# Kernel optimization log

Hardware: AMD Instinct MI355X
Metric: run time of the kernel (lower is better)

The kernel has to match this reference:

```python
import jax, jax.numpy as jnp
import numpy as np

EPS = 1e-5
M = 8          # num_modules
NUM_LAYERS = 4


def gumbel_softmax(logits, u, tau):
    g = -jnp.log(-jnp.log(jnp.clip(u, 1e-10, 1.0 - 1e-7)))
    return jax.nn.softmax((logits + g) / tau, axis=-1)


def batchnorm(x, gamma, beta):
    # training-mode BN over batch axis 0; x: [B, ...], gamma/beta broadcast over trailing dims
    mean = jnp.mean(x, axis=0, keepdims=True)
    var = jnp.mean(jnp.square(x - mean), axis=0, keepdims=True)  # biased var, as torch BN
    return (x - mean) * jax.lax.rsqrt(var + EPS) * gamma + beta


def setup_inputs() -> dict:
    key = jax.random.key(0)
    ks = jax.random.split(key, 32)
    B = 16384
    d = {}
    d['x'] = jax.random.normal(ks[0], (B, 128), jnp.float32)
    d['embedding_input'] = jax.random.normal(ks[1], (B, 128), jnp.float32)
    d['u_sel'] = jax.random.uniform(ks[2], (B, NUM_LAYERS - 1, M, M), jnp.float32)
    d['u_final'] = jax.random.uniform(ks[3], (B, M), jnp.float32)
    shapes = [('base_W0', (128, 400)), ('base_b0', (400,)), ('base_W1', (400, 256)), ('base_b1', (256,)),
              ('em_W0', (128, 400)), ('em_b0', (400,)),
              ('gat_W0', (400, 256)), ('gat_b0', (256,)), ('gat_W1', (256, 256)), ('gat_b1', (256,)),
              ('sel_W', (3, 256, 64)), ('sel_b', (3, 64)), ('selF_W', (256, 8)), ('selF_b', (8,)),
              ('cond_W', (3, 64, 256)), ('cond_b', (3, 256)),
              ('mod_W', (8, 256, 256)), ('mod_b', (8, 256)),
              ('last_W', (256, 18)), ('last_b', (18,))]
    for i, (name, sh) in enumerate(shapes):
        fan_in = sh[-2] if len(sh) >= 2 else sh[-1]
        d[name] = jax.random.normal(ks[4 + i], sh, jnp.float32) / np.sqrt(fan_in)
    d['bn1_g'] = jnp.ones((8, 256), jnp.float32)
    d['bn1_b'] = jnp.zeros((8, 256), jnp.float32)
    d['bn2_g'] = jnp.ones((8, 256), jnp.float32)
    d['bn2_b'] = jnp.zeros((8, 256), jnp.float32)
    return d


def forward(x, embedding_input, u_sel, u_final,
            base_W0, base_b0, base_W1, base_b1, em_W0, em_b0,
            gat_W0, gat_b0, gat_W1, gat_b1,
            sel_W, sel_b, selF_W, selF_b, cond_W, cond_b,
            mod_W, mod_b, bn1_g, bn1_b, bn2_g, bn2_b, last_W, last_b):
    relu = jax.nn.relu
    # base MLP (last activation is identity)
    h = relu(x @ base_W0 + base_b0)
    out = h @ base_W1 + base_b1                       # [B, 256]
    # embedding base (single layer, identity last activation)
    emb = embedding_input @ em_W0 + em_b0             # [B, 400]
    # gating fcs: activation THEN fc, per source loop
    emb = relu(emb) @ gat_W0 + gat_b0
    emb = relu(emb) @ gat_W1 + gat_b1                 # [B, 256]

    # routing logits (stochastic branch, tau = select_temp = 1.0)
    select_input = relu(emb)
    gsels = []
    for i in range(NUM_LAYERS - 1):
        logit = jnp.tanh(select_input @ sel_W[i] + sel_b[i])       # [B, 64]
        sraw = logit.reshape(logit.shape[0], M, M)                  # [B, M, M]
        gsels.append(gumbel_softmax(sraw, u_sel[:, i], 1.0))
        select_input = relu((logit @ cond_W[i] + cond_b[i]) * emb)
    final_select = gumbel_softmax(select_input @ selF_W + selF_b, u_final, 1.0)  # [B, M]
    # selects were insert(0, ...)'d in torch -> consumed in reversed order
    selects = gsels[::-1]

    # layer-0 expert modules: BN -> Linear -> BN (only layers[0] is used in forward)
    mean = jnp.mean(out, axis=0, keepdims=True)
    var = jnp.mean(jnp.square(out - mean), axis=0, keepdims=True)
    xhat = (out - mean) * jax.lax.rsqrt(var + EPS)                  # shared normalization
    t = xhat[:, None, :] * bn1_g + bn1_b                            # [B, M, 256] per-module affine
    h = jnp.einsum('bmd,mdh->bmh', t, mod_W) + mod_b                # [B, M, 256]
    prev = batchnorm(h, bn2_g, bn2_b)                               # [B, M, 256]

    # cascade: weighted combination + relu per layer
    for l in range(NUM_LAYERS - 1):
        prev = relu(jnp.einsum('bmk,bkh->bmh', selects[l], prev))
    out = jnp.einsum('bm,bmh->bh', final_select, prev)              # [B, 256]
    return out @ last_W + last_b                                    # [B, 18]


def reference(x, embedding_input, u_sel, u_final,
              base_W0, base_b0, base_W1, base_b1, em_W0, em_b0,
              gat_W0, gat_b0, gat_W1, gat_b1,
              sel_W, sel_b, selF_W, selF_b, cond_W, cond_b,
              mod_W, mod_b, bn1_g, bn1_b, bn2_g, bn2_b, last_W, last_b):
    return forward(x, embedding_input, u_sel, u_final,
                   base_W0, base_b0, base_W1, base_b1, em_W0, em_b0,
                   gat_W0, gat_b0, gat_W1, gat_b1,
                   sel_W, sel_b, selF_W, selF_b, cond_W, cond_b,
                   mod_W, mod_b, bn1_g, bn1_b, bn2_g, bn2_b, last_W, last_b)
```

## Files before the change

### kernel.cpp

```cpp
#include <hip/hip_runtime.h>
#include <math.h>


typedef short bf16x8 __attribute__((ext_vector_type(8)));
typedef float f32x4 __attribute__((ext_vector_type(4)));

__device__ __forceinline__ unsigned short f2bf(float f) {
  unsigned u = __float_as_uint(f);
  u += 0x7fffu + ((u >> 16) & 1u);
  return (unsigned short)(u >> 16);
}
__device__ __forceinline__ float bf2f(unsigned short h) {
  return __uint_as_float(((unsigned)h) << 16);
}
__device__ __forceinline__ unsigned pack2(float a, float b) {
  return ((unsigned)f2bf(b) << 16) | f2bf(a);
}
__device__ __forceinline__ void gload_lds16(const void* g, void* l) {
  __builtin_amdgcn_global_load_lds(
      (const __attribute__((address_space(1))) unsigned int*)g,
      (__attribute__((address_space(3))) unsigned int*)l, 16, 0, 0);
}
__device__ __forceinline__ bf16x8 relu_bf8(bf16x8 v) {
  bf16x8 r;
  #pragma unroll
  for (int j = 0; j < 8; ++j) r[j] = v[j] > 0 ? v[j] : (short)0;
  return r;
}

#define EPI_NONE  0
#define EPI_RELU  1
#define EPI_STATS 4

__global__ __launch_bounds__(256) void prep_all(
    const float* __restrict__ base_W0, const float* __restrict__ em_W0,
    const float* __restrict__ base_W1, const float* __restrict__ gat_W0,
    const float* __restrict__ gat_W1, const float* __restrict__ sel_W,
    const float* __restrict__ cond_W, const float* __restrict__ last_W,
    unsigned short* __restrict__ W0t, unsigned short* __restrict__ emW0t,
    unsigned short* __restrict__ W1t, unsigned short* __restrict__ g0t,
    unsigned short* __restrict__ g1t, unsigned short* __restrict__ selWt,
    unsigned short* __restrict__ condWt, unsigned short* __restrict__ lastWt,
    float* __restrict__ stats)
{
  __shared__ float t[32][33];
  int bid = blockIdx.x;
  const int tid = threadIdx.x;
  const int tx = tid & 31, ty = tid >> 5;

  if (bid < 496) {
    const float* src; unsigned short* dst; int K, N, KP, gx, local;
    if (bid < 64)       { src = base_W0; dst = W0t;   K = 128; N = 400; KP = 128; gx = 4;  local = bid; }
    else if (bid < 128) { src = em_W0;   dst = emW0t; K = 128; N = 400; KP = 128; gx = 4;  local = bid - 64; }
    else if (bid < 232) { src = base_W1; dst = W1t;   K = 400; N = 256; KP = 416; gx = 13; local = bid - 128; }
    else if (bid < 336) { src = gat_W0;  dst = g0t;   K = 400; N = 256; KP = 416; gx = 13; local = bid - 232; }
    else if (bid < 400) { src = gat_W1;  dst = g1t;   K = 256; N = 256; KP = 256; gx = 8;  local = bid - 336; }
    else if (bid < 448) {
      const int i = (bid - 400) / 16;
      src = sel_W + i * 16384; dst = selWt + i * 16384;
      K = 256; N = 64; KP = 256; gx = 8; local = (bid - 400) % 16;
    } else {
      const int i = (bid - 448) / 16;
      src = cond_W + i * 16384; dst = condWt + i * 16384;
      K = 64; N = 256; KP = 64; gx = 2; local = (bid - 448) % 16;
    }
    const int k0 = (local % gx) * 32, n0 = (local / gx) * 32;
    #pragma unroll
    for (int p = 0; p < 4; ++p) {
      const int k = k0 + ty + p * 8;
      t[ty + p * 8][tx] = (k < K && n0 + tx < N) ? src[(size_t)k * N + n0 + tx] : 0.f;
    }
    __syncthreads();
    #pragma unroll
    for (int p = 0; p < 4; ++p) {
      const int n = n0 + ty + p * 8;
      dst[(size_t)n * KP + k0 + tx] = f2bf(t[tx][ty + p * 8]);
    }
    return;
  }
  bid -= 496;

  if (bid < 8) {
    const int k0 = bid * 32;
    #pragma unroll
    for (int p = 0; p < 4; ++p)
      t[ty + p * 8][tx] = (tx < 18) ? last_W[(size_t)(k0 + ty + p * 8) * 18 + tx] : 0.f;
    __syncthreads();
    #pragma unroll
    for (int p = 0; p < 4; ++p) {
      const int n = ty + p * 8;
      lastWt[(size_t)n * 256 + k0 + tx] = f2bf(t[tx][n]);
      lastWt[(size_t)(n + 32) * 256 + k0 + tx] = 0;
    }
    return;
  }

  for (int i = tid; i < 4608; i += 256) stats[i] = 0.f;
}

__global__ __launch_bounds__(256) void gemm_w0(
    const float* __restrict__ Ax, const float* __restrict__ Ae,
    const unsigned short* __restrict__ Wx, const unsigned short* __restrict__ We,
    const float* __restrict__ bx, const float* __restrict__ be,
    unsigned short* __restrict__ Cx, unsigned short* __restrict__ Ce)
{
  __shared__ unsigned short As[128 * 32];
  __shared__ unsigned short Bs[128 * 32];
  const float* Ap = blockIdx.z ? Ae : Ax;
  const unsigned short* Wp = blockIdx.z ? We : Wx;
  const float* bp = blockIdx.z ? be : bx;
  unsigned short* Cp = blockIdx.z ? Ce : Cx;
  const int row0 = blockIdx.y * 128;
  const int n0 = blockIdx.x * 128;
  const int tid = threadIdx.x;
  const int wid = tid >> 6, lane = tid & 63;
  const int wr = wid >> 1, wc = wid & 1;
  const int arow = tid >> 2, kcol = (tid & 3) * 8;
  const int lr = lane & 15, lk = (lane >> 4) * 8;
  const int lrow = (lane >> 4) * 4;

  f32x4 acc[4][4] = {};
  for (int k0 = 0; k0 < 128; k0 += 32) {
    {
      const float4* s1 = reinterpret_cast<const float4*>(
          Ap + (size_t)(row0 + arow) * 128 + k0 + kcol);
      uint4 w1 = {pack2(s1[0].x, s1[0].y), pack2(s1[0].z, s1[0].w),
                  pack2(s1[1].x, s1[1].y), pack2(s1[1].z, s1[1].w)};
      *reinterpret_cast<uint4*>(&As[arow * 32 + kcol]) = w1;
      const float4* s2 = reinterpret_cast<const float4*>(
          Ap + (size_t)(row0 + 64 + arow) * 128 + k0 + kcol);
      uint4 w2 = {pack2(s2[0].x, s2[0].y), pack2(s2[0].z, s2[0].w),
                  pack2(s2[1].x, s2[1].y), pack2(s2[1].z, s2[1].w)};
      *reinterpret_cast<uint4*>(&As[(64 + arow) * 32 + kcol]) = w2;
    }
    gload_lds16(Wp + (size_t)(n0 + arow) * 128 + k0 + kcol, (char*)Bs + tid * 16);
    gload_lds16(Wp + (size_t)(n0 + 64 + arow) * 128 + k0 + kcol,
                (char*)Bs + 4096 + tid * 16);
    __syncthreads();
    bf16x8 a[4], b[4];
    #pragma unroll
    for (int i = 0; i < 4; ++i)
      a[i] = *reinterpret_cast<const bf16x8*>(&As[(wr * 64 + i * 16 + lr) * 32 + lk]);
    #pragma unroll
    for (int j = 0; j < 4; ++j)
      b[j] = *reinterpret_cast<const bf16x8*>(&Bs[(wc * 64 + j * 16 + lr) * 32 + lk]);
    #pragma unroll
    for (int i = 0; i < 4; ++i)
      #pragma unroll
      for (int j = 0; j < 4; ++j)
        acc[i][j] = __builtin_amdgcn_mfma_f32_16x16x32_bf16(a[i], b[j], acc[i][j], 0, 0, 0);
    __syncthreads();
  }
  #pragma unroll
  for (int j = 0; j < 4; ++j) {
    const int col = n0 + wc * 64 + j * 16 + lr;
    if (col >= 416) continue;
    const bool real = col < 400;
    const float bv = real ? bp[col] : 0.f;
    #pragma unroll
    for (int i = 0; i < 4; ++i) {
      #pragma unroll
      for (int r = 0; r < 4; ++r) {
        const int row = row0 + wr * 64 + i * 16 + lrow + r;
        float v = real ? fmaxf(acc[i][j][r] + bv, 0.f) : 0.f;
        Cp[(size_t)row * 416 + col] = f2bf(v);
      }
    }
  }
}

template<int BN, int WM, int WN, int EPI, bool RELU_A>
__global__ __launch_bounds__(256) void gemm_bf16(
    const unsigned short* __restrict__ A, int AS,
    const unsigned short* __restrict__ Wt, const float* __restrict__ bias,
    unsigned short* __restrict__ C, int CS, int Nreal, int NP, int K,
    const unsigned short* __restrict__ emb,
    float* __restrict__ sum, float* __restrict__ sumsq)
{
  constexpr int FRAG_M = 128 / WM / 16;
  constexpr int FRAG_N = BN / WN / 16;
  __shared__ unsigned short As[128 * 32];
  __shared__ unsigned short Bs[BN * 32];
  const int row0 = blockIdx.y * 128;
  const int n0 = blockIdx.x * BN;
  const int tid = threadIdx.x;
  const int wid = tid >> 6, lane = tid & 63;
  const int wr = wid / WN, wc = wid % WN;
  const int arow = tid >> 2;
  const int kcol = (tid & 3) * 8;
  const int lr = lane & 15, lk = (lane >> 4) * 8;
  const int lrow = (lane >> 4) * 4;

  f32x4 acc[FRAG_M][FRAG_N] = {};
  for (int k0 = 0; k0 < K; k0 += 32) {
    gload_lds16(A + (size_t)(row0 + arow) * AS + k0 + kcol, (char*)As + tid * 16);
    gload_lds16(A + (size_t)(row0 + 64 + arow) * AS + k0 + kcol, (char*)As + 4096 + tid * 16);
    gload_lds16(Wt + (size_t)(n0 + arow) * K + k0 + kcol, (char*)Bs + tid * 16);
    if constexpr (BN == 128)
      gload_lds16(Wt + (size_t)(n0 + 64 + arow) * K + k0 + kcol, (char*)Bs + 4096 + tid * 16);
    __syncthreads();
    bf16x8 a[FRAG_M], b[FRAG_N];
    #pragma unroll
    for (int i = 0; i < FRAG_M; ++i) {
      a[i] = *reinterpret_cast<const bf16x8*>(&As[(wr * (128 / WM) + i * 16 + lr) * 32 + lk]);
      if (RELU_A) a[i] = relu_bf8(a[i]);
    }
    #pragma unroll
    for (int j = 0; j < FRAG_N; ++j)
      b[j] = *reinterpret_cast<const bf16x8*>(&Bs[(wc * (BN / WN) + j * 16 + lr) * 32 + lk]);
    #pragma unroll
    for (int i = 0; i < FRAG_M; ++i)
      #pragma unroll
      for (int j = 0; j < FRAG_N; ++j)
        acc[i][j] = __builtin_amdgcn_mfma_f32_16x16x32_bf16(a[i], b[j], acc[i][j], 0, 0, 0);
    __syncthreads();
  }
  #pragma unroll
  for (int j = 0; j < FRAG_N; ++j) {
    const int col = n0 + wc * (BN / WN) + j * 16 + lr;
    if (col >= NP) continue;
    const bool real = col < Nreal;
    const float bv = real ? bias[col] : 0.f;
    float s = 0.f, q = 0.f;
    #pragma unroll
    for (int i = 0; i < FRAG_M; ++i) {
      #pragma unroll
      for (int r = 0; r < 4; ++r) {
        const int row = row0 + wr * (128 / WM) + i * 16 + lrow + r;
        float v = acc[i][j][r] + bv;
        if (EPI == EPI_RELU) v = fmaxf(v, 0.f);
        if (!real) v = 0.f;
        const unsigned short hv = f2bf(v);
        C[(size_t)row * CS + col] = hv;
        if (EPI == EPI_STATS) {
          const float vr = bf2f(hv);
          s += vr;
          q = fmaf(vr, vr, q);
        }
      }
    }
    if (EPI == EPI_STATS) {
      s += __shfl_xor(s, 16); s += __shfl_xor(s, 32);
      q += __shfl_xor(q, 16); q += __shfl_xor(q, 32);
      if (lane < 16) {
        atomicAdd(&sum[col], s);
        atomicAdd(&sumsq[col], q);
      }
    }
  }
}

__global__ __launch_bounds__(256) void gemm_mod(
    const unsigned short* __restrict__ A,
    const unsigned short* __restrict__ Wt,
    const float* __restrict__ bias, unsigned short* __restrict__ C,
    float* __restrict__ sum, float* __restrict__ sumsq)
{
  __shared__ unsigned short As[128 * 32];
  __shared__ unsigned short Bs[128 * 32];
  const int lin = blockIdx.x;
  const int swz = (lin & 7) * 256 + (lin >> 3);
  const int row0 = (swz >> 4) * 128;
  const int n0 = (swz & 15) * 128;
  const int tid = threadIdx.x;
  const int wid = tid >> 6, lane = tid & 63;
  const int wr = wid >> 1, wc = wid & 1;
  const int arow = tid >> 2;
  const int kcol = (tid & 3) * 8;
  const int lr = lane & 15, lk = (lane >> 4) * 8;
  const int lrow = (lane >> 4) * 4;

  f32x4 acc[4][4] = {};
  for (int k0 = 0; k0 < 256; k0 += 32) {
    gload_lds16(A + (size_t)(row0 + arow) * 256 + k0 + kcol, (char*)As + tid * 16);
    gload_lds16(A + (size_t)(row0 + 64 + arow) * 256 + k0 + kcol, (char*)As + 4096 + tid * 16);
    gload_lds16(Wt + (size_t)(n0 + arow) * 256 + k0 + kcol, (char*)Bs + tid * 16);
    gload_lds16(Wt + (size_t)(n0 + 64 + arow) * 256 + k0 + kcol, (char*)Bs + 4096 + tid * 16);
    __syncthreads();
    bf16x8 a[4], b[4];
    #pragma unroll
    for (int i = 0; i < 4; ++i)
      a[i] = *reinterpret_cast<const bf16x8*>(&As[(wr * 64 + i * 16 + lr) * 32 + lk]);
    #pragma unroll
    for (int j = 0; j < 4; ++j)
      b[j] = *reinterpret_cast<const bf16x8*>(&Bs[(wc * 64 + j * 16 + lr) * 32 + lk]);
    #pragma unroll
    for (int i = 0; i < 4; ++i)
      #pragma unroll
      for (int j = 0; j < 4; ++j)
        acc[i][j] = __builtin_amdgcn_mfma_f32_16x16x32_bf16(a[i], b[j], acc[i][j], 0, 0, 0);
    __syncthreads();
  }
  #pragma unroll
  for (int j = 0; j < 4; ++j) {
    const int col = n0 + wc * 64 + j * 16 + lr;
    const float bv = bias[col];
    float s = 0.f, q = 0.f;
    #pragma unroll
    for (int i = 0; i < 4; ++i) {
      #pragma unroll
      for (int r = 0; r < 4; ++r) {
        const int row = row0 + wr * 64 + i * 16 + lrow + r;
        const unsigned short hv = f2bf(acc[i][j][r] + bv);
        C[(size_t)row * 2048 + col] = hv;
        const float vr = bf2f(hv);
        s += vr;
        q = fmaf(vr, vr, q);
      }
    }
    s += __shfl_xor(s, 16); s += __shfl_xor(s, 32);
    q += __shfl_xor(q, 16); q += __shfl_xor(q, 32);
    if (lane < 16) {
      atomicAdd(&sum[col], s);
      atomicAdd(&sumsq[col], q);
    }
  }
}

template<bool RELU_A>
__global__ __launch_bounds__(256) void fused_select(
    const unsigned short* __restrict__ A, const unsigned short* __restrict__ selWt,
    const float* __restrict__ selb, const unsigned short* __restrict__ condWt,
    const float* __restrict__ condb, const unsigned short* __restrict__ emb,
    const float* __restrict__ u, int u_off,
    float* __restrict__ gs, unsigned short* __restrict__ siout)
{
  __shared__ unsigned short As[128 * 32];
  __shared__ unsigned short Bs[64 * 32];
  __shared__ unsigned short Ls[128 * 72];
  const int tid = threadIdx.x;
  const int wid = tid >> 6, lane = tid & 63;
  const int lr = lane & 15, hi = lane >> 4;
  const int lk = hi * 8;
  const int row0 = blockIdx.x * 128;
  const int arow = tid >> 2, kcol = (tid & 3) * 8;

  {
    f32x4 acc[2][4] = {};
    for (int k0 = 0; k0 < 256; k0 += 32) {
      gload_lds16(A + (size_t)(row0 + arow) * 256 + k0 + kcol, (char*)As + tid * 16);
      gload_lds16(A + (size_t)(row0 + 64 + arow) * 256 + k0 + kcol, (char*)As + 4096 + tid * 16);
      gload_lds16(selWt + (size_t)arow * 256 + k0 + kcol, (char*)Bs + tid * 16);
      __syncthreads();
      bf16x8 a[2], b[4];
      #pragma unroll
      for (int i = 0; i < 2; ++i) {
        a[i] = *reinterpret_cast<const bf16x8*>(&As[(wid * 32 + i * 16 + lr) * 32 + lk]);
        if (RELU_A) a[i] = relu_bf8(a[i]);
      }
      #pragma unroll
      for (int j = 0; j < 4; ++j)
        b[j] = *reinterpret_cast<const bf16x8*>(&Bs[(j * 16 + lr) * 32 + lk]);
      #pragma unroll
      for (int i = 0; i < 2; ++i)
        #pragma unroll
        for (int j = 0; j < 4; ++j)
          acc[i][j] = __builtin_amdgcn_mfma_f32_16x16x32_bf16(a[i], b[j], acc[i][j], 0, 0, 0);
      __syncthreads();
    }
    #pragma unroll
    for (int j = 0; j < 4; ++j) {
      const int col = j * 16 + lr;
      const float bv = selb[col];
      #pragma unroll
      for (int i = 0; i < 2; ++i)
        #pragma unroll
        for (int r = 0; r < 4; ++r) {
          const int row = wid * 32 + i * 16 + hi * 4 + r;
          Ls[row * 72 + col] = f2bf(tanhf(acc[i][j][r] + bv));
        }
    }
  }
  __syncthreads();

  #pragma unroll
  for (int p = 0; p < 4; ++p) {
    const int pair = p * 256 + tid;
    const int bl = pair >> 3, mm = pair & 7;
    const int bg = row0 + bl;
    float v[8];
    #pragma unroll
    for (int jj = 0; jj < 8; ++jj) v[jj] = bf2f(Ls[bl * 72 + mm * 8 + jj]);
    const float* up = u + (size_t)bg * 192 + u_off + mm * 8;
    #pragma unroll
    for (int jj = 0; jj < 8; ++jj) {
      const float uu = fminf(fmaxf(up[jj], 1e-10f), 0.9999999f);
      v[jj] -= logf(-logf(uu));
    }
    float mx = v[0];
    #pragma unroll
    for (int jj = 1; jj < 8; ++jj) mx = fmaxf(mx, v[jj]);
    float s = 0.f;
    #pragma unroll
    for (int jj = 0; jj < 8; ++jj) { v[jj] = expf(v[jj] - mx); s += v[jj]; }
    const float inv = 1.f / s;
    float* op = gs + (size_t)bg * 64 + mm * 8;
    #pragma unroll
    for (int jj = 0; jj < 8; ++jj) op[jj] = v[jj] * inv;
  }

  {
    const int wr2 = wid >> 1, wc2 = wid & 1;
    f32x4 acc2[4][8] = {};
    #pragma unroll
    for (int kq = 0; kq < 2; ++kq) {
      const int k0 = kq * 32;
      bf16x8 a2[4];
      #pragma unroll
      for (int i = 0; i < 4; ++i)
        a2[i] = *reinterpret_cast<const bf16x8*>(
            &Ls[(wr2 * 64 + i * 16 + lr) * 72 + k0 + hi * 8]);
      #pragma unroll
      for (int j = 0; j < 8; ++j) {
        const bf16x8 b2 = *reinterpret_cast<const bf16x8*>(
            condWt + (size_t)(wc2 * 128 + j * 16 + lr) * 64 + k0 + hi * 8);
        #pragma unroll
        for (int i = 0; i < 4; ++i)
          acc2[i][j] = __builtin_amdgcn_mfma_f32_16x16x32_bf16(a2[i], b2, acc2[i][j], 0, 0, 0);
      }
    }
    #pragma unroll
    for (int j = 0; j < 8; ++j) {
      const int col = wc2 * 128 + j * 16 + lr;
      const float bv = condb[col];
      #pragma unroll
      for (int i = 0; i < 4; ++i)
        #pragma unroll
        for (int r = 0; r < 4; ++r) {
          const int row = row0 + wr2 * 64 + i * 16 + hi * 4 + r;
          float vv = (acc2[i][j][r] + bv) * bf2f(emb[(size_t)row * 256 + col]);
          siout[(size_t)row * 256 + col] = f2bf(fmaxf(vv, 0.f));
        }
    }
  }
}

__global__ void final_select_k(const unsigned short* __restrict__ si, const float* __restrict__ Wf,
                               const float* __restrict__ bias, const float* __restrict__ u,
                               float* __restrict__ fs)
{
  const int idx = blockIdx.x * 256 + threadIdx.x;
  const int b = idx >> 3, j = idx & 7;
  const unsigned short* sp = si + (size_t)b * 256;
  float acc = bias[j];
  for (int k = 0; k < 256; ++k) acc = fmaf(bf2f(sp[k]), Wf[k * 8 + j], acc);
  const float uu = fminf(fmaxf(u[(size_t)b * 8 + j], 1e-10f), 0.9999999f);
  float v = acc - logf(-logf(uu));
  float mx = v;
  #pragma unroll
  for (int d = 1; d < 8; d <<= 1) mx = fmaxf(mx, __shfl_xor(mx, d, 8));
  float e = expf(v - mx);
  float s = e;
  #pragma unroll
  for (int d = 1; d < 8; d <<= 1) s += __shfl_xor(s, d, 8);
  fs[(size_t)b * 8 + j] = e / s;
}

__global__ __launch_bounds__(256) void fold_modw_all(
    const float* __restrict__ W, const float* __restrict__ g1,
    const float* __restrict__ b1, const float* __restrict__ modb,
    const float* __restrict__ sum1, const float* __restrict__ sumsq1,
    unsigned short* __restrict__ Wt, float* __restrict__ bias2)
{
  const float invB = 1.f / 16384.f;
  if (blockIdx.z == 8) {
    if (blockIdx.y != 0) return;
    const int m = blockIdx.x, h = threadIdx.x;
    float acc = modb[m * 256 + h];
    for (int d = 0; d < 256; ++d) {
      const float mean = sum1[d] * invB;
      const float var = sumsq1[d] * invB - mean * mean;
      const float r = rsqrtf(var + 1e-5f);
      const float c = b1[m * 256 + d] - mean * r * g1[m * 256 + d];
      acc = fmaf(c, W[((size_t)m * 256 + d) * 256 + h], acc);
    }
    bias2[m * 256 + h] = acc;
    return;
  }
  __shared__ float t[32][33];
  const int m = blockIdx.z, d0 = blockIdx.y * 32, h0 = blockIdx.x * 32;
  const int tx = threadIdx.x & 31, ty = threadIdx.x >> 5;
  #pragma unroll
  for (int p = 0; p < 4; ++p) {
    const int d = d0 + ty + p * 8;
    const float mean = sum1[d] * invB;
    const float var = sumsq1[d] * invB - mean * mean;
    const float r = rsqrtf(var + 1e-5f);
    t[ty + p * 8][tx] = W[((size_t)m * 256 + d) * 256 + h0 + tx] * r * g1[m * 256 + d];
  }
  __syncthreads();
  #pragma unroll
  for (int p = 0; p < 4; ++p) {
    const int h = h0 + ty + p * 8;
    Wt[((size_t)m * 256 + h) * 256 + d0 + tx] = f2bf(t[tx][ty + p * 8]);
  }
}

__global__ void finalize_bn2(const float* __restrict__ sum, const float* __restrict__ sumsq,
                             const float* __restrict__ g, const float* __restrict__ b,
                             float* __restrict__ scale, float* __restrict__ shift)
{
  const int i = blockIdx.x * 256 + threadIdx.x;
  const float invB = 1.f / 16384.f;
  const float m = sum[i] * invB;
  const float v = sumsq[i] * invB - m * m;
  const float r = rsqrtf(v + 1e-5f);
  const float sc = r * g[i];
  scale[i] = sc;
  shift[i] = b[i] - m * sc;
}

__global__ __launch_bounds__(256) void final_cascade(
    const unsigned short* __restrict__ H, const float* __restrict__ scale2,
    const float* __restrict__ shift2, const float* __restrict__ gs0,
    const float* __restrict__ gs1, const float* __restrict__ gs2,
    const float* __restrict__ fs, unsigned short* __restrict__ ovec)
{
  const int wave = threadIdx.x >> 6, lane = threadIdx.x & 63;
  const int b = __builtin_amdgcn_readfirstlane(blockIdx.x * 4 + wave);
  const int c0 = lane << 2;

  float prev[8][4];
  #pragma unroll
  for (int m = 0; m < 8; ++m) {
    const int gc = m * 256 + c0;
    const ushort4 h = *reinterpret_cast<const ushort4*>(&H[(size_t)b * 2048 + gc]);
    const float4 sc = *reinterpret_cast<const float4*>(&scale2[gc]);
    const float4 sh = *reinterpret_cast<const float4*>(&shift2[gc]);
    prev[m][0] = bf2f(h.x) * sc.x + sh.x;
    prev[m][1] = bf2f(h.y) * sc.y + sh.y;
    prev[m][2] = bf2f(h.z) * sc.z + sh.z;
    prev[m][3] = bf2f(h.w) * sc.w + sh.w;
  }

  const float* sel0 = gs2 + (size_t)b * 64;
  const float* sel1 = gs1 + (size_t)b * 64;
  const float* sel2 = gs0 + (size_t)b * 64;
  #pragma unroll
  for (int l = 0; l < 3; ++l) {
    const float* sp = (l == 0) ? sel0 : (l == 1) ? sel1 : sel2;
    float nw[8][4];
    #pragma unroll
    for (int m = 0; m < 8; ++m) {
      float a0 = 0.f, a1 = 0.f, a2 = 0.f, a3 = 0.f;
      #pragma unroll
      for (int k = 0; k < 8; ++k) {
        const float s = sp[m * 8 + k];
        a0 = fmaf(s, prev[k][0], a0);
        a1 = fmaf(s, prev[k][1], a1);
        a2 = fmaf(s, prev[k][2], a2);
        a3 = fmaf(s, prev[k][3], a3);
      }
      nw[m][0] = fmaxf(a0, 0.f); nw[m][1] = fmaxf(a1, 0.f);
      nw[m][2] = fmaxf(a2, 0.f); nw[m][3] = fmaxf(a3, 0.f);
    }
    #pragma unroll
    for (int m = 0; m < 8; ++m)
      #pragma unroll
      for (int c = 0; c < 4; ++c)
        prev[m][c] = nw[m][c];
  }

  const float* fp = fs + (size_t)b * 8;
  float ov[4] = {0.f, 0.f, 0.f, 0.f};
  #pragma unroll
  for (int m = 0; m < 8; ++m) {
    const float s = fp[m];
    ov[0] = fmaf(s, prev[m][0], ov[0]);
    ov[1] = fmaf(s, prev[m][1], ov[1]);
    ov[2] = fmaf(s, prev[m][2], ov[2]);
    ov[3] = fmaf(s, prev[m][3], ov[3]);
  }
  ushort4 o;
  o.x = f2bf(ov[0]); o.y = f2bf(ov[1]); o.z = f2bf(ov[2]); o.w = f2bf(ov[3]);
  *reinterpret_cast<ushort4*>(&ovec[(size_t)b * 256 + c0]) = o;
}

__global__ __launch_bounds__(256) void gemm_last(
    const unsigned short* __restrict__ A, const unsigned short* __restrict__ Wt,
    const float* __restrict__ bias, float* __restrict__ out)
{
  __shared__ unsigned short As[128 * 32];
  __shared__ unsigned short Bs[64 * 32];
  const int row0 = blockIdx.y * 128;
  const int tid = threadIdx.x;
  const int wid = tid >> 6, lane = tid & 63;
  const int arow = tid >> 2;
  const int kcol = (tid & 3) * 8;
  const int lr = lane & 15, lk = (lane >> 4) * 8;
  const int lrow = (lane >> 4) * 4;

  f32x4 acc[2][4] = {};
  for (int k0 = 0; k0 < 256; k0 += 32) {
    gload_lds16(A + (size_t)(row0 + arow) * 256 + k0 + kcol, (char*)As + tid * 16);
    gload_lds16(A + (size_t)(row0 + 64 + arow) * 256 + k0 + kcol, (char*)As + 4096 + tid * 16);
    gload_lds16(Wt + (size_t)arow * 256 + k0 + kcol, (char*)Bs + tid * 16);
    __syncthreads();
    bf16x8 a[2], b[4];
    #pragma unroll
    for (int i = 0; i < 2; ++i)
      a[i] = *reinterpret_cast<const bf16x8*>(&As[(wid * 32 + i * 16 + lr) * 32 + lk]);
    #pragma unroll
    for (int j = 0; j < 4; ++j)
      b[j] = *reinterpret_cast<const bf16x8*>(&Bs[(j * 16 + lr) * 32 + lk]);
    #pragma unroll
    for (int i = 0; i < 2; ++i)
      #pragma unroll
      for (int j = 0; j < 4; ++j)
        acc[i][j] = __builtin_amdgcn_mfma_f32_16x16x32_bf16(a[i], b[j], acc[i][j], 0, 0, 0);
    __syncthreads();
  }
  #pragma unroll
  for (int j = 0; j < 2; ++j) {
    const int col = j * 16 + lr;
    if (col >= 18) continue;
    const float bv = bias[col];
    #pragma unroll
    for (int i = 0; i < 2; ++i) {
      #pragma unroll
      for (int r = 0; r < 4; ++r) {
        const int row = row0 + wid * 32 + i * 16 + lrow + r;
        out[(size_t)row * 18 + col] = acc[i][j][r] + bv;
      }
    }
  }
}

extern "C" void kernel_launch(void* const* d_in, const int* in_sizes, int n_in,
                              void* d_out, int out_size, void* d_ws, size_t ws_size,
                              hipStream_t stream)
{
  (void)in_sizes; (void)n_in; (void)out_size; (void)ws_size;
  const float* x       = (const float*)d_in[0];
  const float* embi    = (const float*)d_in[1];
  const float* u_sel   = (const float*)d_in[2];
  const float* u_fin   = (const float*)d_in[3];
  const float* base_W0 = (const float*)d_in[4];
  const float* base_b0 = (const float*)d_in[5];
  const float* base_W1 = (const float*)d_in[6];
  const float* base_b1 = (const float*)d_in[7];
  const float* em_W0   = (const float*)d_in[8];
  const float* em_b0   = (const float*)d_in[9];
  const float* gat_W0  = (const float*)d_in[10];
  const float* gat_b0  = (const float*)d_in[11];
  const float* gat_W1  = (const float*)d_in[12];
  const float* gat_b1  = (const float*)d_in[13];
  const float* sel_W   = (const float*)d_in[14];
  const float* sel_b   = (const float*)d_in[15];
  const float* selF_W  = (const float*)d_in[16];
  const float* selF_b  = (const float*)d_in[17];
  const float* cond_W  = (const float*)d_in[18];
  const float* cond_b  = (const float*)d_in[19];
  const float* mod_W   = (const float*)d_in[20];
  const float* mod_b   = (const float*)d_in[21];
  const float* last_W  = (const float*)d_in[22];
  const float* last_b  = (const float*)d_in[23];
  const float* bn1_g   = (const float*)d_in[24];
  const float* bn1_b   = (const float*)d_in[25];
  const float* bn2_g   = (const float*)d_in[26];
  const float* bn2_b   = (const float*)d_in[27];

  char* WSB = (char*)d_ws;
  unsigned short* h_big    = (unsigned short*)(WSB + 0);
  unsigned short* h1e      = (unsigned short*)(WSB + 67108864);
  unsigned short* ovec_bf  = (unsigned short*)(WSB + 67108864);
  unsigned short* h1       = (unsigned short*)(WSB + 81000448);
  unsigned short* emb_bf   = (unsigned short*)(WSB + 103020544);
  unsigned short* si_bf    = (unsigned short*)(WSB + 111409152);
  unsigned short* out_bf   = (unsigned short*)(WSB + 119797760);
  float* gs0   = (float*)(WSB + 130283520);
  float* gs1   = (float*)(WSB + 134477824);
  float* gs2   = (float*)(WSB + 138672128);
  float* bufFs = (float*)(WSB + 142866432);
  unsigned short* W0t   = (unsigned short*)(WSB + 143390720);
  unsigned short* emW0t = (unsigned short*)(WSB + 143521792);
  unsigned short* W1t   = (unsigned short*)(WSB + 143652864);
  unsigned short* g0t   = (unsigned short*)(WSB + 143865856);
  unsigned short* g1t   = (unsigned short*)(WSB + 144078848);
  unsigned short* selWt = (unsigned short*)(WSB + 144209920);
  unsigned short* condWt= (unsigned short*)(WSB + 144308224);
  unsigned short* modWt = (unsigned short*)(WSB + 144406528);
  float* bias2  = (float*)(WSB + 146503680);
  float* stats  = (float*)(WSB + 146511872);
  unsigned short* lastWt = (unsigned short*)(WSB + 146530304);
  float* scale2 = (float*)(WSB + 146563072);
  float* shift2 = (float*)(WSB + 146571264);
  float* sum1   = stats;        float* sumsq1 = stats + 256;
  float* sum2   = stats + 512;  float* sumsq2 = stats + 2560;

  const dim3 blk(256);
  prep_all<<<dim3(505), blk, 0, stream>>>(
      base_W0, em_W0, base_W1, gat_W0, gat_W1, sel_W, cond_W, last_W,
      W0t, emW0t, W1t, g0t, g1t, selWt, condWt, lastWt, stats);

  gemm_w0<<<dim3(4, 128, 2), blk, 0, stream>>>(
      x, embi, W0t, emW0t, base_b0, em_b0, h1, h1e);
  gemm_bf16<64, 4, 1, EPI_STATS, false><<<dim3(4, 128), blk, 0, stream>>>(
      h1, 416, W1t, base_b1, out_bf, 256, 256, 256, 416, nullptr, sum1, sumsq1);
  gemm_bf16<64, 4, 1, EPI_RELU, false><<<dim3(4, 128), blk, 0, stream>>>(
      h1e, 416, g0t, gat_b0, si_bf, 256, 256, 256, 416, nullptr, nullptr, nullptr);
  gemm_bf16<64, 4, 1, EPI_NONE, false><<<dim3(4, 128), blk, 0, stream>>>(
      si_bf, 256, g1t, gat_b1, emb_bf, 256, 256, 256, 256, nullptr, nullptr, nullptr);
  fused_select<true><<<dim3(128), blk, 0, stream>>>(
      emb_bf, selWt, sel_b, condWt, cond_b, emb_bf, u_sel, 0, gs0, si_bf);
  fused_select<false><<<dim3(128), blk, 0, stream>>>(
      si_bf, selWt + 16384, sel_b + 64, condWt + 16384, cond_b + 256, emb_bf,
      u_sel, 64, gs1, si_bf);
  fused_select<false><<<dim3(128), blk, 0, stream>>>(
      si_bf, selWt + 32768, sel_b + 128, condWt + 32768, cond_b + 512, emb_bf,
      u_sel, 128, gs2, si_bf);
  final_select_k<<<dim3(512), blk, 0, stream>>>(si_bf, selF_W, selF_b, u_fin, bufFs);
  fold_modw_all<<<dim3(8, 8, 9), blk, 0, stream>>>(
      mod_W, bn1_g, bn1_b, mod_b, sum1, sumsq1, modWt, bias2);
  gemm_mod<<<dim3(2048), blk, 0, stream>>>(out_bf, modWt, bias2, h_big, sum2, sumsq2);
  finalize_bn2<<<dim3(8), blk, 0, stream>>>(sum2, sumsq2, bn2_g, bn2_b, scale2, shift2);
  final_cascade<<<dim3(4096), blk, 0, stream>>>(
      h_big, scale2, shift2, gs0, gs1, gs2, bufFs, ovec_bf);
  gemm_last<<<dim3(1, 128), blk, 0, stream>>>(ovec_bf, lastWt, last_b, (float*)d_out);
}
```

Measured before the change: 256.6 us.

## Merge mid GEMMs, swizzle gemm_mod LDS with staged stores, MFMA final select

Three independent changes. The two 416-K GEMMs (base_W1 with BN stats, gat_W0 with relu) are merged into one launch via blockIdx.z. gemm_mod gets an XOR-swizzled LDS layout to cut bank conflicts, and its output is staged through shared memory for coalesced 16-byte global stores. The scalar final_select kernel is replaced by an MFMA GEMM against a bf16-transposed selF_W prepared in prep_all, with the Gumbel-softmax done in the epilogue. This adds LDS use in gemm_mod, which may lower occupancy.

```diff
diff --git a/kernel.cpp b/kernel.cpp
--- a/kernel.cpp
+++ b/kernel.cpp
@@ -37,11 +37,12 @@
     const float* __restrict__ base_W1, const float* __restrict__ gat_W0,
     const float* __restrict__ gat_W1, const float* __restrict__ sel_W,
     const float* __restrict__ cond_W, const float* __restrict__ last_W,
+    const float* __restrict__ selF_W,
     unsigned short* __restrict__ W0t, unsigned short* __restrict__ emW0t,
     unsigned short* __restrict__ W1t, unsigned short* __restrict__ g0t,
     unsigned short* __restrict__ g1t, unsigned short* __restrict__ selWt,
     unsigned short* __restrict__ condWt, unsigned short* __restrict__ lastWt,
-    float* __restrict__ stats)
+    unsigned short* __restrict__ selFt, float* __restrict__ stats)
 {
   __shared__ float t[32][33];
   int bid = blockIdx.x;
@@ -94,6 +95,16 @@
     }
     return;
   }
+  bid -= 8;
+
+  if (bid == 0) {
+    const int k = tid;
+    #pragma unroll
+    for (int j = 0; j < 8; ++j) selFt[j * 256 + k] = f2bf(selF_W[k * 8 + j]);
+    #pragma unroll
+    for (int j = 8; j < 16; ++j) selFt[j * 256 + k] = 0;
+    return;
+  }
 
   for (int i = tid; i < 4608; i += 256) stats[i] = 0.f;
 }
@@ -169,6 +180,80 @@
   }
 }
 
+__global__ __launch_bounds__(256) void gemm_mid(
+    const unsigned short* __restrict__ A0, const unsigned short* __restrict__ W0,
+    const float* __restrict__ b0, unsigned short* __restrict__ C0,
+    const unsigned short* __restrict__ A1, const unsigned short* __restrict__ W1,
+    const float* __restrict__ b1, unsigned short* __restrict__ C1,
+    float* __restrict__ sum, float* __restrict__ sumsq)
+{
+  __shared__ unsigned short As[128 * 32];
+  __shared__ unsigned short Bs[64 * 32];
+  const bool z1 = blockIdx.z != 0;
+  const unsigned short* A = z1 ? A1 : A0;
+  const unsigned short* Wt = z1 ? W1 : W0;
+  const float* bias = z1 ? b1 : b0;
+  unsigned short* C = z1 ? C1 : C0;
+  const int row0 = blockIdx.y * 128;
+  const int n0 = blockIdx.x * 64;
+  const int tid = threadIdx.x;
+  const int wid = tid >> 6, lane = tid & 63;
+  const int arow = tid >> 2, kcol = (tid & 3) * 8;
+  const int lr = lane & 15, lk = (lane >> 4) * 8;
+  const int lrow = (lane >> 4) * 4;
+
+  f32x4 acc[2][4] = {};
+  for (int k0 = 0; k0 < 416; k0 += 32) {
+    gload_lds16(A + (size_t)(row0 + arow) * 416 + k0 + kcol, (char*)As + tid * 16);
+    gload_lds16(A + (size_t)(row0 + 64 + arow) * 416 + k0 + kcol, (char*)As + 4096 + tid * 16);
+    gload_lds16(Wt + (size_t)(n0 + arow) * 416 + k0 + kcol, (char*)Bs + tid * 16);
+    __syncthreads();
+    bf16x8 a[2], b[4];
+    #pragma unroll
+    for (int i = 0; i < 2; ++i)
+      a[i] = *reinterpret_cast<const bf16x8*>(&As[(wid * 32 + i * 16 + lr) * 32 + lk]);
+    #pragma unroll
+    for (int j = 0; j < 4; ++j)
+      b[j] = *reinterpret_cast<const bf16x8*>(&Bs[(j * 16 + lr) * 32 + lk]);
+    #pragma unroll
+    for (int i = 0; i < 2; ++i)
+      #pragma unroll
+      for (int j = 0; j < 4; ++j)
+        acc[i][j] = __builtin_amdgcn_mfma_f32_16x16x32_bf16(a[i], b[j], acc[i][j], 0, 0, 0);
+    __syncthreads();
+  }
+  #pragma unroll
+  for (int j = 0; j < 4; ++j) {
+    const int col = n0 + j * 16 + lr;
+    const float bv = bias[col];
+    float s = 0.f, q = 0.f;
+    #pragma unroll
+    for (int i = 0; i < 2; ++i) {
+      #pragma unroll
+      for (int r = 0; r < 4; ++r) {
+        const int row = row0 + wid * 32 + i * 16 + lrow + r;
+        float v = acc[i][j][r] + bv;
+        if (z1) v = fmaxf(v, 0.f);
+        const unsigned short hv = f2bf(v);
+        C[(size_t)row * 256 + col] = hv;
+        if (!z1) {
+          const float vr = bf2f(hv);
+          s += vr;
+          q = fmaf(vr, vr, q);
+        }
+      }
+    }
+    if (!z1) {
+      s += __shfl_xor(s, 16); s += __shfl_xor(s, 32);
+      q += __shfl_xor(q, 16); q += __shfl_xor(q, 32);
+      if (lane < 16) {
+        atomicAdd(&sum[col], s);
+        atomicAdd(&sumsq[col], q);
+      }
+    }
+  }
+}
+
 template<int BN, int WM, int WN, int EPI, bool RELU_A>
 __global__ __launch_bounds__(256) void gemm_bf16(
     const unsigned short* __restrict__ A, int AS,
@@ -258,6 +343,7 @@
 {
   __shared__ unsigned short As[128 * 32];
   __shared__ unsigned short Bs[128 * 32];
+  __shared__ unsigned short Cs[128 * 136];
   const int lin = blockIdx.x;
   const int swz = (lin & 7) * 256 + (lin >> 3);
   const int row0 = (swz >> 4) * 128;
@@ -266,24 +352,25 @@
   const int wid = tid >> 6, lane = tid & 63;
   const int wr = wid >> 1, wc = wid & 1;
   const int arow = tid >> 2;
-  const int kcol = (tid & 3) * 8;
-  const int lr = lane & 15, lk = (lane >> 4) * 8;
-  const int lrow = (lane >> 4) * 4;
+  const int lr = lane & 15, hi = lane >> 4;
+  const int s_lr = (lr + (lr >> 2)) & 3;
+  const int cswz = ((tid & 3) ^ ((arow + (arow >> 2)) & 3)) * 8;
 
   f32x4 acc[4][4] = {};
   for (int k0 = 0; k0 < 256; k0 += 32) {
-    gload_lds16(A + (size_t)(row0 + arow) * 256 + k0 + kcol, (char*)As + tid * 16);
-    gload_lds16(A + (size_t)(row0 + 64 + arow) * 256 + k0 + kcol, (char*)As + 4096 + tid * 16);
-    gload_lds16(Wt + (size_t)(n0 + arow) * 256 + k0 + kcol, (char*)Bs + tid * 16);
-    gload_lds16(Wt + (size_t)(n0 + 64 + arow) * 256 + k0 + kcol, (char*)Bs + 4096 + tid * 16);
-    __syncthreads();
+    gload_lds16(A + (size_t)(row0 + arow) * 256 + k0 + cswz, (char*)As + tid * 16);
+    gload_lds16(A + (size_t)(row0 + 64 + arow) * 256 + k0 + cswz, (char*)As + 4096 + tid * 16);
+    gload_lds16(Wt + (size_t)(n0 + arow) * 256 + k0 + cswz, (char*)Bs + tid * 16);
+    gload_lds16(Wt + (size_t)(n0 + 64 + arow) * 256 + k0 + cswz, (char*)Bs + 4096 + tid * 16);
+    __syncthreads();
+    const int rchunk = (hi ^ s_lr) * 8;
     bf16x8 a[4], b[4];
     #pragma unroll
     for (int i = 0; i < 4; ++i)
-      a[i] = *reinterpret_cast<const bf16x8*>(&As[(wr * 64 + i * 16 + lr) * 32 + lk]);
+      a[i] = *reinterpret_cast<const bf16x8*>(&As[(wr * 64 + i * 16 + lr) * 32 + rchunk]);
     #pragma unroll
     for (int j = 0; j < 4; ++j)
-      b[j] = *reinterpret_cast<const bf16x8*>(&Bs[(wc * 64 + j * 16 + lr) * 32 + lk]);
+      b[j] = *reinterpret_cast<const bf16x8*>(&Bs[(wc * 64 + j * 16 + lr) * 32 + rchunk]);
     #pragma unroll
     for (int i = 0; i < 4; ++i)
       #pragma unroll
@@ -291,6 +378,7 @@
         acc[i][j] = __builtin_amdgcn_mfma_f32_16x16x32_bf16(a[i], b[j], acc[i][j], 0, 0, 0);
     __syncthreads();
   }
+
   #pragma unroll
   for (int j = 0; j < 4; ++j) {
     const int col = n0 + wc * 64 + j * 16 + lr;
@@ -300,9 +388,8 @@
     for (int i = 0; i < 4; ++i) {
       #pragma unroll
       for (int r = 0; r < 4; ++r) {
-        const int row = row0 + wr * 64 + i * 16 + lrow + r;
         const unsigned short hv = f2bf(acc[i][j][r] + bv);
-        C[(size_t)row * 2048 + col] = hv;
+        Cs[(wr * 64 + i * 16 + hi * 4 + r) * 136 + wc * 64 + j * 16 + lr] = hv;
         const float vr = bf2f(hv);
         s += vr;
         q = fmaf(vr, vr, q);
@@ -313,6 +400,19 @@
     if (lane < 16) {
       atomicAdd(&sum[col], s);
       atomicAdd(&sumsq[col], q);
+    }
+  }
+  __syncthreads();
+  const int colbase = n0;
+  const int qrow = tid >> 2;
+  const int qc = (((tid & 3) ^ qrow) & 3) * 32;
+  #pragma unroll
+  for (int pass = 0; pass < 2; ++pass) {
+    const int row = pass * 64 + qrow;
+    #pragma unroll
+    for (int v = 0; v < 4; ++v) {
+      const uint4 d = *reinterpret_cast<const uint4*>(&Cs[row * 136 + qc + v * 8]);
+      *reinterpret_cast<uint4*>(&C[(size_t)(row0 + row) * 2048 + colbase + qc + v * 8]) = d;
     }
   }
 }
@@ -435,25 +535,60 @@
   }
 }
 
-__global__ void final_select_k(const unsigned short* __restrict__ si, const float* __restrict__ Wf,
-                               const float* __restrict__ bias, const float* __restrict__ u,
-                               float* __restrict__ fs)
-{
-  const int idx = blockIdx.x * 256 + threadIdx.x;
-  const int b = idx >> 3, j = idx & 7;
-  const unsigned short* sp = si + (size_t)b * 256;
-  float acc = bias[j];
-  for (int k = 0; k < 256; ++k) acc = fmaf(bf2f(sp[k]), Wf[k * 8 + j], acc);
-  const float uu = fminf(fmaxf(u[(size_t)b * 8 + j], 1e-10f), 0.9999999f);
-  float v = acc - logf(-logf(uu));
-  float mx = v;
-  #pragma unroll
-  for (int d = 1; d < 8; d <<= 1) mx = fmaxf(mx, __shfl_xor(mx, d, 8));
-  float e = expf(v - mx);
-  float s = e;
-  #pragma unroll
-  for (int d = 1; d < 8; d <<= 1) s += __shfl_xor(s, d, 8);
-  fs[(size_t)b * 8 + j] = e / s;
+__global__ __launch_bounds__(256) void gemm_fsel(
+    const unsigned short* __restrict__ A, const unsigned short* __restrict__ Wt,
+    const float* __restrict__ bias, const float* __restrict__ u,
+    float* __restrict__ fs)
+{
+  __shared__ unsigned short As[128 * 32];
+  __shared__ unsigned short Bs[16 * 32];
+  const int row0 = blockIdx.y * 128;
+  const int tid = threadIdx.x;
+  const int wid = tid >> 6, lane = tid & 63;
+  const int arow = tid >> 2, kcol = (tid & 3) * 8;
+  const int lr = lane & 15, hi = lane >> 4;
+  const int lk = hi * 8;
+
+  f32x4 acc[2] = {};
+  for (int k0 = 0; k0 < 256; k0 += 32) {
+    gload_lds16(A + (size_t)(row0 + arow) * 256 + k0 + kcol, (char*)As + tid * 16);
+    gload_lds16(A + (size_t)(row0 + 64 + arow) * 256 + k0 + kcol, (char*)As + 4096 + tid * 16);
+    if (wid == 0)
+      gload_lds16(Wt + (size_t)(lane >> 2) * 256 + k0 + (lane & 3) * 8, (char*)Bs + lane * 16);
+    __syncthreads();
+    bf16x8 a[2];
+    #pragma unroll
+    for (int i = 0; i < 2; ++i)
+      a[i] = *reinterpret_cast<const bf16x8*>(&As[(wid * 32 + i * 16 + lr) * 32 + lk]);
+    const bf16x8 b = *reinterpret_cast<const bf16x8*>(&Bs[lr * 32 + lk]);
+    #pragma unroll
+    for (int i = 0; i < 2; ++i)
+      acc[i] = __builtin_amdgcn_mfma_f32_16x16x32_bf16(a[i], b, acc[i], 0, 0, 0);
+    __syncthreads();
+  }
+  const float bv = (lr < 8) ? bias[lr] : 0.f;
+  #pragma unroll
+  for (int i = 0; i < 2; ++i) {
+    #pragma unroll
+    for (int r = 0; r < 4; ++r) {
+      const int row = row0 + wid * 32 + i * 16 + hi * 4 + r;
+      float v = acc[i][r] + bv;
+      if (lr < 8) {
+        const float uu = fminf(fmaxf(u[(size_t)row * 8 + lr], 1e-10f), 0.9999999f);
+        v -= logf(-logf(uu));
+      }
+      float mx = v;
+      mx = fmaxf(mx, __shfl_xor(mx, 1));
+      mx = fmaxf(mx, __shfl_xor(mx, 2));
+      mx = fmaxf(mx, __shfl_xor(mx, 4));
+      const float e = expf(v - mx);
+      float ssum = e;
+      ssum += __shfl_xor(ssum, 1);
+      ssum += __shfl_xor(ssum, 2);
+      ssum += __shfl_xor(ssum, 4);
+      if (lr < 8) fs[(size_t)row * 8 + lr] = e / ssum;
+    }
+  }
 }
 
 __global__ __launch_bounds__(256) void fold_modw_all(
@@ -685,20 +820,19 @@
   unsigned short* lastWt = (unsigned short*)(WSB + 146530304);
   float* scale2 = (float*)(WSB + 146563072);
   float* shift2 = (float*)(WSB + 146571264);
+  unsigned short* selFt = (unsigned short*)(WSB + 146579456);
   float* sum1   = stats;        float* sumsq1 = stats + 256;
   float* sum2   = stats + 512;  float* sumsq2 = stats + 2560;
 
   const dim3 blk(256);
-  prep_all<<<dim3(505), blk, 0, stream>>>(
-      base_W0, em_W0, base_W1, gat_W0, gat_W1, sel_W, cond_W, last_W,
-      W0t, emW0t, W1t, g0t, g1t, selWt, condWt, lastWt, stats);
+  prep_all<<<dim3(506), blk, 0, stream>>>(
+      base_W0, em_W0, base_W1, gat_W0, gat_W1, sel_W, cond_W, last_W, selF_W,
+      W0t, emW0t, W1t, g0t, g1t, selWt, condWt, lastWt, selFt, stats);
 
   gemm_w0<<<dim3(4, 128, 2), blk, 0, stream>>>(
       x, embi, W0t, emW0t, base_b0, em_b0, h1, h1e);
-  gemm_bf16<64, 4, 1, EPI_STATS, false><<<dim3(4, 128), blk, 0, stream>>>(
-      h1, 416, W1t, base_b1, out_bf, 256, 256, 256, 416, nullptr, sum1, sumsq1);
-  gemm_bf16<64, 4, 1, EPI_RELU, false><<<dim3(4, 128), blk, 0, stream>>>(
-      h1e, 416, g0t, gat_b0, si_bf, 256, 256, 256, 416, nullptr, nullptr, nullptr);
+  gemm_mid<<<dim3(4, 128, 2), blk, 0, stream>>>(
+      h1, W1t, base_b1, out_bf, h1e, g0t, gat_b0, si_bf, sum1, sumsq1);
   gemm_bf16<64, 4, 1, EPI_NONE, false><<<dim3(4, 128), blk, 0, stream>>>(
       si_bf, 256, g1t, gat_b1, emb_bf, 256, 256, 256, 256, nullptr, nullptr, nullptr);
   fused_select<true><<<dim3(128), blk, 0, stream>>>(
@@ -709,7 +843,7 @@
   fused_select<false><<<dim3(128), blk, 0, stream>>>(
       si_bf, selWt + 32768, sel_b + 128, condWt + 32768, cond_b + 512, emb_bf,
       u_sel, 128, gs2, si_bf);
-  final_select_k<<<dim3(512), blk, 0, stream>>>(si_bf, selF_W, selF_b, u_fin, bufFs);
+  gemm_fsel<<<dim3(1, 128), blk, 0, stream>>>(si_bf, selFt, selF_b, u_fin, bufFs);
   fold_modw_all<<<dim3(8, 8, 9), blk, 0, stream>>>(
       mod_W, bn1_g, bn1_b, mod_b, sum1, sumsq1, modWt, bias2);
   gemm_mod<<<dim3(2048), blk, 0, stream>>>(out_bf, modWt, bias2, h_big, sum2, sumsq2);
```

After: 254.9 us. Within noise of the previous version (-0.7%).
